# Kernel tuning notes

Measured on AMD Instinct MI355X. Metric: run time of the kernel, lower is better.

## Reference

```python
import jax, jax.numpy as jnp
import numpy as np

N_NODES = 50000
N_EDGES = 800000
D = 64


def setup_inputs() -> dict:
    key = jax.random.key(0)
    k1, k2, k3, k4, k5 = jax.random.split(key, 5)
    feat = jax.random.normal(k1, (N_NODES, D), dtype=jnp.float32)
    h_e = jax.random.normal(k2, (1, D), dtype=jnp.float32)
    W = jax.random.normal(k3, (D, D), dtype=jnp.float32) * (1.0 / np.sqrt(D))
    src = jax.random.randint(k4, (N_EDGES,), 0, N_NODES, dtype=jnp.int32)
    dst = jax.random.randint(k5, (N_EDGES,), 0, N_NODES, dtype=jnp.int32)
    return {"feat": feat, "h_e": h_e, "W": W, "src": src, "dst": dst}


def reference(feat, h_e, W, src, dst):
    # CompConv with comp_fn='sub', norm='right', linear=True, no bias/activation.
    n_nodes = feat.shape[0]
    # edge gather + compose: comp_h[e] = feat[src[e]] - h_e  (E, D)
    comp_h = feat[src] - h_e
    # shared linear transform on edge messages (E, D_out)
    m = comp_h @ W
    # scatter-sum messages to destination nodes (N, D_out)
    rst = jax.ops.segment_sum(m, dst, num_segments=n_nodes)
    # 'right' norm: divide by in-degree (clamped to >= 1)
    degs = jax.ops.segment_sum(jnp.ones_like(dst, dtype=jnp.float32), dst,
                               num_segments=n_nodes)
    degs = jnp.maximum(degs, 1.0)
    return rst / degs[:, None]
```

## Files before the change

kernel.cpp:

```cpp
#include <hip/hip_runtime.h>

#define DIM 64
#define NPB 64
#define NPB_LOG 6
#define MAXNB 1024
#define ECAP 2048

typedef unsigned short ushort_t;
typedef float f32x4 __attribute__((ext_vector_type(4)));


__device__ __forceinline__ ushort_t f2bf_rne(float f) {
    const unsigned u = __float_as_uint(f);
    return (ushort_t)((u + 0x7FFFu + ((u >> 16) & 1u)) >> 16);
}

__global__ void __launch_bounds__(256)
cc_prep(const float* __restrict__ feat, ushort_t* __restrict__ featb,
        int n_elems, int* __restrict__ ccnt) {
    if (blockIdx.x == 0)
        for (int i = threadIdx.x; i < MAXNB; i += 256) ccnt[i] = 0;
    int i = (blockIdx.x * blockDim.x + threadIdx.x) * 4;
    const int stride = gridDim.x * blockDim.x * 4;
    for (; i + 3 < n_elems; i += stride) {
        const float4 v = *(const float4*)&feat[i];
        ushort4 o;
        o.x = f2bf_rne(v.x); o.y = f2bf_rne(v.y);
        o.z = f2bf_rne(v.z); o.w = f2bf_rne(v.w);
        *(ushort4*)&featb[i] = o;
    }
}

__global__ void __launch_bounds__(256)
cc_count(const int* __restrict__ dst, int* __restrict__ ccnt, int n_edges, int nb) {
    __shared__ int lc[MAXNB];
    for (int i = threadIdx.x; i < nb; i += 256) lc[i] = 0;
    __syncthreads();
    int i = blockIdx.x * blockDim.x + threadIdx.x;
    const int stride = gridDim.x * blockDim.x;
    for (; i < n_edges; i += stride)
        atomicAdd(&lc[dst[i] >> NPB_LOG], 1);
    __syncthreads();
    for (int i = threadIdx.x; i < nb; i += 256)
        if (lc[i]) atomicAdd(&ccnt[i], lc[i]);
}

__global__ void __launch_bounds__(256)
cc_scan(const int* __restrict__ ccnt, int* __restrict__ coff, int* __restrict__ ccur,
        int nb) {
    __shared__ int wsum[4];
    const int tid = threadIdx.x, lane = tid & 63, wid = tid >> 6;
    const int i0 = tid * 4;
    const int v0 = (i0     < nb) ? ccnt[i0]     : 0;
    const int v1 = (i0 + 1 < nb) ? ccnt[i0 + 1] : 0;
    const int v2 = (i0 + 2 < nb) ? ccnt[i0 + 2] : 0;
    const int v3 = (i0 + 3 < nb) ? ccnt[i0 + 3] : 0;
    const int tt = v0 + v1 + v2 + v3;
    int incl = tt;
    for (int off = 1; off < 64; off <<= 1) {
        const int u = __shfl_up(incl, off, 64);
        if (lane >= off) incl += u;
    }
    if (lane == 63) wsum[wid] = incl;
    __syncthreads();
    int wbase = 0;
    for (int w = 0; w < wid; ++w) wbase += wsum[w];
    const int ex = wbase + incl - tt;
    if (i0     < nb) { coff[i0]     = ex;                ccur[i0]     = ex; }
    if (i0 + 1 < nb) { coff[i0 + 1] = ex + v0;           ccur[i0 + 1] = ex + v0; }
    if (i0 + 2 < nb) { coff[i0 + 2] = ex + v0 + v1;      ccur[i0 + 2] = ex + v0 + v1; }
    if (i0 + 3 < nb) { coff[i0 + 3] = ex + v0 + v1 + v2; ccur[i0 + 3] = ex + v0 + v1 + v2; }
    if (tid == 255) coff[nb] = wbase + incl;
}

__global__ void __launch_bounds__(256)
cc_scatter(const int* __restrict__ src, const int* __restrict__ dst,
           int* __restrict__ ccur, int* __restrict__ packed,
           int n_edges, int nb) {
    __shared__ int lc[MAXNB];
    __shared__ int lbase[MAXNB];
    const int ch = (n_edges + gridDim.x - 1) / gridDim.x;
    const int lo = blockIdx.x * ch;
    const int hi = min(lo + ch, n_edges);
    for (int i = threadIdx.x; i < nb; i += 256) lc[i] = 0;
    __syncthreads();
    for (int i = lo + threadIdx.x; i < hi; i += 256)
        atomicAdd(&lc[dst[i] >> NPB_LOG], 1);
    __syncthreads();
    for (int i = threadIdx.x; i < nb; i += 256) {
        const int c = lc[i];
        lbase[i] = c ? atomicAdd(&ccur[i], c) : 0;
        lc[i] = 0;
    }
    __syncthreads();
    for (int i = lo + threadIdx.x; i < hi; i += 256) {
        const int d = dst[i];
        const int b = d >> NPB_LOG;
        const int p = lbase[b] + atomicAdd(&lc[b], 1);
        packed[p] = (int)(((unsigned)d << 16) | (unsigned)src[i]);
    }
}

#define ADD8(a, q)                                          \
    {                                                       \
        a[0] += __uint_as_float((q).x << 16);               \
        a[1] += __uint_as_float((q).x & 0xFFFF0000u);       \
        a[2] += __uint_as_float((q).y << 16);               \
        a[3] += __uint_as_float((q).y & 0xFFFF0000u);       \
        a[4] += __uint_as_float((q).z << 16);               \
        a[5] += __uint_as_float((q).z & 0xFFFF0000u);       \
        a[6] += __uint_as_float((q).w << 16);               \
        a[7] += __uint_as_float((q).w & 0xFFFF0000u);       \
    }

__global__ void __launch_bounds__(256)
cc_fused(const ushort_t* __restrict__ featb, const float* __restrict__ Wg,
         const float* __restrict__ h_e, const int* __restrict__ coff,
         const int* __restrict__ packed, float* __restrict__ out, int n_nodes) {
    __shared__ float Wl[DIM * DIM];
    __shared__ float At[NPB][DIM + 4];
    __shared__ int   esl_in[ECAP];
    __shared__ int   esl[ECAP];
    __shared__ int   deg[NPB];
    __shared__ int   loff[NPB];
    __shared__ int   cur[NPB];
    __shared__ float heWl[DIM];

    const int t   = threadIdx.x;
    const int b   = blockIdx.x;
    const int e0  = coff[b];
    const int cnt = coff[b + 1] - e0;
    const bool fits = (cnt <= ECAP);

    for (int i = t * 4; i < DIM * DIM; i += 1024)
        *(float4*)&Wl[i] = *(const float4*)&Wg[i];
    if (t < NPB) deg[t] = 0;
    __syncthreads();

    for (int i = t; i < cnt; i += 256) {
        const int pk = packed[e0 + i];
        if (fits) esl_in[i] = pk;
        atomicAdd(&deg[(((unsigned)pk) >> 16) & (NPB - 1)], 1);
    }
    __syncthreads();

    if (t < 64) {
        const int v = deg[t];
        int incl = v;
        for (int off = 1; off < 64; off <<= 1) {
            const int u = __shfl_up(incl, off, 64);
            if (t >= off) incl += u;
        }
        loff[t] = incl - v;
        cur[t]  = 0;
    } else if (t < 128) {
        const int c = t - 64;
        float s = 0.f;
        for (int k = 0; k < DIM; ++k) s += h_e[k] * Wl[k * DIM + c];
        heWl[c] = s;
    }
    __syncthreads();

    if (fits) {
        for (int i = t; i < cnt; i += 256) {
            const int pk = esl_in[i];
            const int l  = (((unsigned)pk) >> 16) & (NPB - 1);
            esl[loff[l] + atomicAdd(&cur[l], 1)] = pk & 0xFFFF;
        }
    }
    __syncthreads();

    const int grp = t >> 3;
    const int dq  = t & 7;
#pragma unroll
    for (int half = 0; half < 2; ++half) {
        const int l  = grp + half * 32;
        const int d0 = loff[l];
        const int dn = deg[l];
        float a[8] = {0.f, 0.f, 0.f, 0.f, 0.f, 0.f, 0.f, 0.f};
        if (fits) {
            int e = 0;
            for (; e + 2 <= dn; e += 2) {
                const int s0 = esl[d0 + e];
                const int s1 = esl[d0 + e + 1];
                const uint4 q0 = *(const uint4*)&featb[(size_t)s0 * DIM + dq * 8];
                const uint4 q1 = *(const uint4*)&featb[(size_t)s1 * DIM + dq * 8];
                ADD8(a, q0);
                ADD8(a, q1);
            }
            if (e < dn) {
                const int s = esl[d0 + e];
                const uint4 q = *(const uint4*)&featb[(size_t)s * DIM + dq * 8];
                ADD8(a, q);
            }
        } else {
            for (int i = 0; i < cnt; ++i) {
                const int pk = packed[e0 + i];
                if ((int)((((unsigned)pk) >> 16) & (NPB - 1)) == l) {
                    const uint4 q =
                        *(const uint4*)&featb[(size_t)(pk & 0xFFFF) * DIM + dq * 8];
                    ADD8(a, q);
                }
            }
        }
        const f32x4 v0 = {a[0], a[1], a[2], a[3]};
        const f32x4 v1 = {a[4], a[5], a[6], a[7]};
        *(f32x4*)&At[l][dq * 8]     = v0;
        *(f32x4*)&At[l][dq * 8 + 4] = v1;
    }
    __syncthreads();

    const int tx = t & 15, ty = t >> 4;
    float acc[4][4] = {{0.f}};
#pragma unroll 8
    for (int k = 0; k < DIM; ++k) {
        const float4 bv = *(const float4*)&Wl[k * DIM + tx * 4];
        const float a0 = At[ty * 4 + 0][k];
        const float a1 = At[ty * 4 + 1][k];
        const float a2 = At[ty * 4 + 2][k];
        const float a3 = At[ty * 4 + 3][k];
        acc[0][0] += a0 * bv.x; acc[0][1] += a0 * bv.y; acc[0][2] += a0 * bv.z; acc[0][3] += a0 * bv.w;
        acc[1][0] += a1 * bv.x; acc[1][1] += a1 * bv.y; acc[1][2] += a1 * bv.z; acc[1][3] += a1 * bv.w;
        acc[2][0] += a2 * bv.x; acc[2][1] += a2 * bv.y; acc[2][2] += a2 * bv.z; acc[2][3] += a2 * bv.w;
        acc[3][0] += a3 * bv.x; acc[3][1] += a3 * bv.y; acc[3][2] += a3 * bv.z; acc[3][3] += a3 * bv.w;
    }
    const float hw0 = heWl[tx * 4 + 0], hw1 = heWl[tx * 4 + 1];
    const float hw2 = heWl[tx * 4 + 2], hw3 = heWl[tx * 4 + 3];
    const int n0 = b << NPB_LOG;
#pragma unroll
    for (int i = 0; i < 4; ++i) {
        const int n = n0 + ty * 4 + i;
        if (n < n_nodes) {
            const float dg = (float)deg[ty * 4 + i];
            const float rd = 1.0f / fmaxf(dg, 1.0f);
            float4 o;
            o.x = (acc[i][0] - dg * hw0) * rd;
            o.y = (acc[i][1] - dg * hw1) * rd;
            o.z = (acc[i][2] - dg * hw2) * rd;
            o.w = (acc[i][3] - dg * hw3) * rd;
            *(float4*)&out[(size_t)n * DIM + tx * 4] = o;
        }
    }
}

__global__ void __launch_bounds__(256)
compconv_hist(const int* __restrict__ dst, int* __restrict__ deg_i, int n_edges) {
    int i = blockIdx.x * blockDim.x + threadIdx.x;
    const int stride = gridDim.x * blockDim.x;
    for (; i < n_edges; i += stride)
        atomicAdd(&deg_i[dst[i]], 1);
}

__global__ void __launch_bounds__(1024)
compconv_scan1(const int* __restrict__ deg_i, int* __restrict__ offsets,
               int* __restrict__ cursor, int n) {
    __shared__ int wsum[16];
    __shared__ int s_carry;
    const int tid = threadIdx.x, lane = tid & 63, wid = tid >> 6;
    if (tid == 0) s_carry = 0;
    __syncthreads();
    const int CHUNK = 1024 * 4;
    for (int base = 0; base < n; base += CHUNK) {
        const int idx = base + tid * 4;
        int4 v = make_int4(0, 0, 0, 0);
        if (idx + 3 < n) v = *(const int4*)&deg_i[idx];
        else {
            if (idx + 0 < n) v.x = deg_i[idx + 0];
            if (idx + 1 < n) v.y = deg_i[idx + 1];
            if (idx + 2 < n) v.z = deg_i[idx + 2];
            if (idx + 3 < n) v.w = deg_i[idx + 3];
        }
        const int t = v.x + v.y + v.z + v.w;
        int incl = t;
        for (int off = 1; off < 64; off <<= 1) {
            const int u = __shfl_up(incl, off, 64);
            if (lane >= off) incl += u;
        }
        if (lane == 63) wsum[wid] = incl;
        __syncthreads();
        if (wid == 0) {
            const int w = (lane < 16) ? wsum[lane] : 0;
            int winc = w;
            for (int off = 1; off < 16; off <<= 1) {
                const int u = __shfl_up(winc, off, 64);
                if (lane >= off) winc += u;
            }
            if (lane < 16) wsum[lane] = winc - w;
        }
        __syncthreads();
        const int ex = s_carry + wsum[wid] + (incl - t);
        if (idx + 3 < n) {
            const int4 ov = make_int4(ex, ex + v.x, ex + v.x + v.y, ex + v.x + v.y + v.z);
            *(int4*)&offsets[idx] = ov;
            *(int4*)&cursor[idx]  = ov;
        } else {
            if (idx + 0 < n) { offsets[idx+0] = ex;               cursor[idx+0] = offsets[idx+0]; }
            if (idx + 1 < n) { offsets[idx+1] = ex+v.x;           cursor[idx+1] = offsets[idx+1]; }
            if (idx + 2 < n) { offsets[idx+2] = ex+v.x+v.y;       cursor[idx+2] = offsets[idx+2]; }
            if (idx + 3 < n) { offsets[idx+3] = ex+v.x+v.y+v.z;   cursor[idx+3] = offsets[idx+3]; }
        }
        __syncthreads();
        if (tid == 1023) s_carry = ex + t;
        __syncthreads();
    }
    if (tid == 0) offsets[n] = s_carry;
}

__global__ void __launch_bounds__(256)
compconv_bucket(const int* __restrict__ src, const int* __restrict__ dst,
                int* __restrict__ cursor, int* __restrict__ edge_src, int n_edges) {
    int i = blockIdx.x * blockDim.x + threadIdx.x;
    const int stride = gridDim.x * blockDim.x;
    for (; i < n_edges; i += stride) {
        const int p = atomicAdd(&cursor[dst[i]], 1);
        edge_src[p] = src[i];
    }
}

__global__ void __launch_bounds__(256)
compconv_gather(const float* __restrict__ feat, const float* __restrict__ Wg,
                const float* __restrict__ h_e, const int* __restrict__ offsets,
                const int* __restrict__ edge_src, float* __restrict__ out,
                int n_nodes) {
    __shared__ float Wl[DIM * DIM];
    for (int i = threadIdx.x * 4; i < DIM * DIM; i += blockDim.x * 4)
        *(float4*)&Wl[i] = *(const float4*)&Wg[i];
    __syncthreads();

    const int lane = threadIdx.x & 63;
    const int g    = lane >> 4;
    const int dq   = lane & 15;

    const float he = h_e[lane];
    float heW = 0.0f;
#pragma unroll
    for (int k = 0; k < DIM; ++k)
        heW += __shfl(he, k, 64) * Wl[k * DIM + lane];

    const int wave   = (blockIdx.x * blockDim.x + threadIdx.x) >> 6;
    const int nwaves = (gridDim.x * blockDim.x) >> 6;
    for (int n = wave; n < n_nodes; n += nwaves) {
        const int e0 = offsets[n];
        const int e1 = offsets[n + 1];
        float ax = 0.0f, ay = 0.0f, az = 0.0f, aw = 0.0f;
        int e = e0;
        for (; e + 8 <= e1; e += 8) {
            const int s0 = edge_src[e + g];
            const int s1 = edge_src[e + 4 + g];
            const float4 a = *(const float4*)&feat[(size_t)s0 * DIM + dq * 4];
            const float4 b = *(const float4*)&feat[(size_t)s1 * DIM + dq * 4];
            ax += a.x + b.x; ay += a.y + b.y; az += a.z + b.z; aw += a.w + b.w;
        }
        if (e + 4 <= e1) {
            const int s = edge_src[e + g];
            const float4 a = *(const float4*)&feat[(size_t)s * DIM + dq * 4];
            ax += a.x; ay += a.y; az += a.z; aw += a.w;
            e += 4;
        }
        if (g < e1 - e) {
            const int s = edge_src[e + g];
            const float4 a = *(const float4*)&feat[(size_t)s * DIM + dq * 4];
            ax += a.x; ay += a.y; az += a.z; aw += a.w;
        }
        ax += __shfl_xor(ax, 16, 64); ay += __shfl_xor(ay, 16, 64);
        az += __shfl_xor(az, 16, 64); aw += __shfl_xor(aw, 16, 64);
        ax += __shfl_xor(ax, 32, 64); ay += __shfl_xor(ay, 32, 64);
        az += __shfl_xor(az, 32, 64); aw += __shfl_xor(aw, 32, 64);

        float s = 0.0f;
#pragma unroll
        for (int q = 0; q < 16; ++q) {
            const float a0 = __shfl(ax, q, 64);
            const float a1 = __shfl(ay, q, 64);
            const float a2 = __shfl(az, q, 64);
            const float a3 = __shfl(aw, q, 64);
            s += a0 * Wl[(4 * q + 0) * DIM + lane]
               + a1 * Wl[(4 * q + 1) * DIM + lane]
               + a2 * Wl[(4 * q + 2) * DIM + lane]
               + a3 * Wl[(4 * q + 3) * DIM + lane];
        }
        const float dg = (float)(e1 - e0);
        out[(size_t)n * DIM + lane] = (s - dg * heW) / fmaxf(dg, 1.0f);
    }
}

extern "C" void kernel_launch(void* const* d_in, const int* in_sizes, int n_in,
                              void* d_out, int out_size, void* d_ws, size_t ws_size,
                              hipStream_t stream) {
    const float* feat = (const float*)d_in[0];
    const float* h_e  = (const float*)d_in[1];
    const float* W    = (const float*)d_in[2];
    const int*   src  = (const int*)d_in[3];
    const int*   dst  = (const int*)d_in[4];

    const int n_edges = in_sizes[3];
    const int n_nodes = in_sizes[0] / DIM;

    float* out = (float*)d_out;

    const int nb   = (n_nodes + NPB - 1) >> NPB_LOG;
    const int epad = (n_edges + 3) & ~3;

    const size_t need = ((size_t)(1024 + 1024 + 1028) + epad) * sizeof(int) +
                        (size_t)n_nodes * DIM * sizeof(ushort_t);
    const bool primary_ok = (n_nodes <= 65536) && (nb <= MAXNB) && (ws_size >= need);

    if (primary_ok) {
        int* ccnt   = (int*)d_ws;
        int* ccur   = ccnt + 1024;
        int* coff   = ccur + 1024;
        int* packed = coff + 1028;
        ushort_t* featb = (ushort_t*)(packed + epad);

        cc_prep   <<<1024, 256, 0, stream>>>(feat, featb, n_nodes * DIM, ccnt);
        cc_count  <<<256,  256, 0, stream>>>(dst, ccnt, n_edges, nb);
        cc_scan   <<<1,    256, 0, stream>>>(ccnt, coff, ccur, nb);
        cc_scatter<<<256,  256, 0, stream>>>(src, dst, ccur, packed, n_edges, nb);
        cc_fused  <<<nb,   256, 0, stream>>>(featb, W, h_e, coff, packed, out, n_nodes);
    } else {
        int* deg_i    = (int*)d_ws;
        int* cursor   = deg_i + n_nodes;
        int* offsets  = cursor + n_nodes;
        int* edge_src = offsets + (n_nodes + 1);

        hipMemsetAsync(deg_i, 0, (size_t)n_nodes * sizeof(int), stream);
        compconv_hist<<<1024, 256, 0, stream>>>(dst, deg_i, n_edges);
        compconv_scan1<<<1, 1024, 0, stream>>>(deg_i, offsets, cursor, n_nodes);
        compconv_bucket<<<1024, 256, 0, stream>>>(src, dst, cursor, edge_src, n_edges);
        compconv_gather<<<2048, 256, 0, stream>>>(feat, W, h_e, offsets, edge_src,
                                                  out, n_nodes);
    }
}
```

Measured before the change: 77.43 us.

## Fuse count into prep and scan into scatter, shrink LDS edge list

Merges the destination-bucket histogram into the bf16 conversion kernel and folds the single-block scan into every scatter block, so each block recomputes the prefix sum redundantly instead of running a separate launch. This cuts the pipeline from five kernels to three plus a memset. In the fused gather kernel, the edge list in shared memory becomes 16-bit and the staging copy is removed, so packed is reread from global memory. The gather loop is also unrolled to four loads. The trade-off is redundant scan work in each of the 256 scatter blocks and a second global read of packed.

```diff
diff --git a/kernel.cpp b/kernel.cpp
--- a/kernel.cpp
+++ b/kernel.cpp
@@ -16,29 +16,23 @@
 }
 
 __global__ void __launch_bounds__(256)
-cc_prep(const float* __restrict__ feat, ushort_t* __restrict__ featb,
-        int n_elems, int* __restrict__ ccnt) {
-    if (blockIdx.x == 0)
-        for (int i = threadIdx.x; i < MAXNB; i += 256) ccnt[i] = 0;
-    int i = (blockIdx.x * blockDim.x + threadIdx.x) * 4;
-    const int stride = gridDim.x * blockDim.x * 4;
-    for (; i + 3 < n_elems; i += stride) {
+cc_prep2(const float* __restrict__ feat, ushort_t* __restrict__ featb, int n_elems,
+         const int* __restrict__ dst, int n_edges, int* __restrict__ ccnt, int nb) {
+    __shared__ int lc[MAXNB];
+    for (int i = threadIdx.x; i < nb; i += 256) lc[i] = 0;
+    __syncthreads();
+
+    const int gid    = blockIdx.x * blockDim.x + threadIdx.x;
+    const int stride = gridDim.x * blockDim.x;
+
+    for (int i = gid * 4; i + 3 < n_elems; i += stride * 4) {
         const float4 v = *(const float4*)&feat[i];
         ushort4 o;
         o.x = f2bf_rne(v.x); o.y = f2bf_rne(v.y);
         o.z = f2bf_rne(v.z); o.w = f2bf_rne(v.w);
         *(ushort4*)&featb[i] = o;
     }
-}
-
-__global__ void __launch_bounds__(256)
-cc_count(const int* __restrict__ dst, int* __restrict__ ccnt, int n_edges, int nb) {
-    __shared__ int lc[MAXNB];
-    for (int i = threadIdx.x; i < nb; i += 256) lc[i] = 0;
-    __syncthreads();
-    int i = blockIdx.x * blockDim.x + threadIdx.x;
-    const int stride = gridDim.x * blockDim.x;
-    for (; i < n_edges; i += stride)
+    for (int i = gid; i < n_edges; i += stride)
         atomicAdd(&lc[dst[i] >> NPB_LOG], 1);
     __syncthreads();
     for (int i = threadIdx.x; i < nb; i += 256)
@@ -46,10 +40,16 @@
 }
 
 __global__ void __launch_bounds__(256)
-cc_scan(const int* __restrict__ ccnt, int* __restrict__ coff, int* __restrict__ ccur,
-        int nb) {
+cc_scatter2(const int* __restrict__ src, const int* __restrict__ dst,
+            const int* __restrict__ ccnt, int* __restrict__ ccur,
+            int* __restrict__ coff_g, int* __restrict__ packed,
+            int n_edges, int nb) {
+    __shared__ int lc[MAXNB];
+    __shared__ int lbase[MAXNB];
+    __shared__ int coffs[MAXNB + 4];
     __shared__ int wsum[4];
     const int tid = threadIdx.x, lane = tid & 63, wid = tid >> 6;
+
     const int i0 = tid * 4;
     const int v0 = (i0     < nb) ? ccnt[i0]     : 0;
     const int v1 = (i0 + 1 < nb) ? ccnt[i0 + 1] : 0;
@@ -66,34 +66,30 @@
     int wbase = 0;
     for (int w = 0; w < wid; ++w) wbase += wsum[w];
     const int ex = wbase + incl - tt;
-    if (i0     < nb) { coff[i0]     = ex;                ccur[i0]     = ex; }
-    if (i0 + 1 < nb) { coff[i0 + 1] = ex + v0;           ccur[i0 + 1] = ex + v0; }
-    if (i0 + 2 < nb) { coff[i0 + 2] = ex + v0 + v1;      ccur[i0 + 2] = ex + v0 + v1; }
-    if (i0 + 3 < nb) { coff[i0 + 3] = ex + v0 + v1 + v2; ccur[i0 + 3] = ex + v0 + v1 + v2; }
-    if (tid == 255) coff[nb] = wbase + incl;
-}
-
-__global__ void __launch_bounds__(256)
-cc_scatter(const int* __restrict__ src, const int* __restrict__ dst,
-           int* __restrict__ ccur, int* __restrict__ packed,
-           int n_edges, int nb) {
-    __shared__ int lc[MAXNB];
-    __shared__ int lbase[MAXNB];
+    if (i0     < nb) coffs[i0]     = ex;
+    if (i0 + 1 < nb) coffs[i0 + 1] = ex + v0;
+    if (i0 + 2 < nb) coffs[i0 + 2] = ex + v0 + v1;
+    if (i0 + 3 < nb) coffs[i0 + 3] = ex + v0 + v1 + v2;
+    if (tid == 255) coffs[nb] = wbase + incl;
+    for (int i = tid; i < nb; i += 256) lc[i] = 0;
+    __syncthreads();
+
+    if (blockIdx.x == 0)
+        for (int i = tid; i <= nb; i += 256) coff_g[i] = coffs[i];
+
     const int ch = (n_edges + gridDim.x - 1) / gridDim.x;
     const int lo = blockIdx.x * ch;
     const int hi = min(lo + ch, n_edges);
-    for (int i = threadIdx.x; i < nb; i += 256) lc[i] = 0;
-    __syncthreads();
-    for (int i = lo + threadIdx.x; i < hi; i += 256)
+    for (int i = lo + tid; i < hi; i += 256)
         atomicAdd(&lc[dst[i] >> NPB_LOG], 1);
     __syncthreads();
-    for (int i = threadIdx.x; i < nb; i += 256) {
+    for (int i = tid; i < nb; i += 256) {
         const int c = lc[i];
-        lbase[i] = c ? atomicAdd(&ccur[i], c) : 0;
+        lbase[i] = c ? (coffs[i] + atomicAdd(&ccur[i], c)) : 0;
         lc[i] = 0;
     }
     __syncthreads();
-    for (int i = lo + threadIdx.x; i < hi; i += 256) {
+    for (int i = lo + tid; i < hi; i += 256) {
         const int d = dst[i];
         const int b = d >> NPB_LOG;
         const int p = lbase[b] + atomicAdd(&lc[b], 1);
@@ -114,17 +110,16 @@
     }
 
 __global__ void __launch_bounds__(256)
-cc_fused(const ushort_t* __restrict__ featb, const float* __restrict__ Wg,
-         const float* __restrict__ h_e, const int* __restrict__ coff,
-         const int* __restrict__ packed, float* __restrict__ out, int n_nodes) {
-    __shared__ float Wl[DIM * DIM];
-    __shared__ float At[NPB][DIM + 4];
-    __shared__ int   esl_in[ECAP];
-    __shared__ int   esl[ECAP];
-    __shared__ int   deg[NPB];
-    __shared__ int   loff[NPB];
-    __shared__ int   cur[NPB];
-    __shared__ float heWl[DIM];
+cc_fused2(const ushort_t* __restrict__ featb, const float* __restrict__ Wg,
+          const float* __restrict__ h_e, const int* __restrict__ coff,
+          const int* __restrict__ packed, float* __restrict__ out, int n_nodes) {
+    __shared__ float    Wl[DIM * DIM];
+    __shared__ float    At[NPB][DIM + 4];
+    __shared__ ushort_t esl[ECAP];
+    __shared__ int      deg[NPB];
+    __shared__ int      loff[NPB];
+    __shared__ int      cur[NPB];
+    __shared__ float    heWl[DIM];
 
     const int t   = threadIdx.x;
     const int b   = blockIdx.x;
@@ -137,11 +132,8 @@
     if (t < NPB) deg[t] = 0;
     __syncthreads();
 
-    for (int i = t; i < cnt; i += 256) {
-        const int pk = packed[e0 + i];
-        if (fits) esl_in[i] = pk;
-        atomicAdd(&deg[(((unsigned)pk) >> 16) & (NPB - 1)], 1);
-    }
+    for (int i = t; i < cnt; i += 256)
+        atomicAdd(&deg[(((unsigned)packed[e0 + i]) >> 16) & (NPB - 1)], 1);
     __syncthreads();
 
     if (t < 64) {
@@ -163,9 +155,9 @@
 
     if (fits) {
         for (int i = t; i < cnt; i += 256) {
-            const int pk = esl_in[i];
+            const int pk = packed[e0 + i];
             const int l  = (((unsigned)pk) >> 16) & (NPB - 1);
-            esl[loff[l] + atomicAdd(&cur[l], 1)] = pk & 0xFFFF;
+            esl[loff[l] + atomicAdd(&cur[l], 1)] = (ushort_t)(pk & 0xFFFF);
         }
     }
     __syncthreads();
@@ -180,15 +172,21 @@
         float a[8] = {0.f, 0.f, 0.f, 0.f, 0.f, 0.f, 0.f, 0.f};
         if (fits) {
             int e = 0;
-            for (; e + 2 <= dn; e += 2) {
+            for (; e + 4 <= dn; e += 4) {
                 const int s0 = esl[d0 + e];
                 const int s1 = esl[d0 + e + 1];
+                const int s2 = esl[d0 + e + 2];
+                const int s3 = esl[d0 + e + 3];
                 const uint4 q0 = *(const uint4*)&featb[(size_t)s0 * DIM + dq * 8];
                 const uint4 q1 = *(const uint4*)&featb[(size_t)s1 * DIM + dq * 8];
+                const uint4 q2 = *(const uint4*)&featb[(size_t)s2 * DIM + dq * 8];
+                const uint4 q3 = *(const uint4*)&featb[(size_t)s3 * DIM + dq * 8];
                 ADD8(a, q0);
                 ADD8(a, q1);
+                ADD8(a, q2);
+                ADD8(a, q3);
             }
-            if (e < dn) {
+            for (; e < dn; ++e) {
                 const int s = esl[d0 + e];
                 const uint4 q = *(const uint4*)&featb[(size_t)s * DIM + dq * 8];
                 ADD8(a, q);
@@ -412,11 +410,13 @@
         int* packed = coff + 1028;
         ushort_t* featb = (ushort_t*)(packed + epad);
 
-        cc_prep   <<<1024, 256, 0, stream>>>(feat, featb, n_nodes * DIM, ccnt);
-        cc_count  <<<256,  256, 0, stream>>>(dst, ccnt, n_edges, nb);
-        cc_scan   <<<1,    256, 0, stream>>>(ccnt, coff, ccur, nb);
-        cc_scatter<<<256,  256, 0, stream>>>(src, dst, ccur, packed, n_edges, nb);
-        cc_fused  <<<nb,   256, 0, stream>>>(featb, W, h_e, coff, packed, out, n_nodes);
+        hipMemsetAsync(ccnt, 0, 2048 * sizeof(int), stream);
+        cc_prep2   <<<1024, 256, 0, stream>>>(feat, featb, n_nodes * DIM,
+                                              dst, n_edges, ccnt, nb);
+        cc_scatter2<<<256,  256, 0, stream>>>(src, dst, ccnt, ccur, coff,
+                                              packed, n_edges, nb);
+        cc_fused2  <<<nb,   256, 0, stream>>>(featb, W, h_e, coff, packed,
+                                              out, n_nodes);
     } else {
         int* deg_i    = (int*)d_ws;
         int* cursor   = deg_i + n_nodes;
```

New measurement: 83.60 us. 8.0% more time.
